# Optimization experiments

Hardware: AMD Instinct MI355X
Metric: run time of the kernel (lower is better)

The kernel has to match this reference:

```python
import jax, jax.numpy as jnp
import numpy as np

LEVEL = 2
INV_SQRT2 = 0.7071067811865476
# subband order: index 0 is the approx (x_coeff1[0]); the 7 details match the
# {'aad','ada','add','daa','dad','dda','ddd'} dict keys of wavedec3 level-`LEVEL`.
SUBS = ['aaa', 'aad', 'ada', 'add', 'daa', 'dad', 'dda', 'ddd']


def dwt1(x, axis):
    # single-level Haar (db1, periodic) analysis along one axis
    x = jnp.moveaxis(x, axis, -1)
    n = x.shape[-1]
    x = x.reshape(*x.shape[:-1], n // 2, 2)
    a = (x[..., 0] + x[..., 1]) * INV_SQRT2
    d = (x[..., 0] - x[..., 1]) * INV_SQRT2
    return jnp.moveaxis(a, -1, axis), jnp.moveaxis(d, -1, axis)


def dwt3(x):
    # separable 3D Haar DWT over the last 3 axes -> 8 subbands keyed 'aaa'..'ddd'
    subs = {'': x}
    for axis in (-3, -2, -1):
        nxt = {}
        for k, v in subs.items():
            a, d = dwt1(v, axis)
            nxt[k + 'a'] = a
            nxt[k + 'd'] = d
        subs = nxt
    return subs


def idwt1(a, d, axis):
    a = jnp.moveaxis(a, axis, -1)
    d = jnp.moveaxis(d, axis, -1)
    x = jnp.stack([(a + d) * INV_SQRT2, (a - d) * INV_SQRT2], axis=-1)
    x = x.reshape(*x.shape[:-2], x.shape[-2] * 2)
    return jnp.moveaxis(x, -1, axis)


def idwt3(subs):
    for axis in (-1, -2, -3):
        prefixes = sorted(set(k[:-1] for k in subs))
        subs = {p: idwt1(subs[p + 'a'], subs[p + 'd'], axis) for p in prefixes}
    return subs['']


def upsample_zero_details(a):
    # one inverse-DWT level with all detail coeffs = 0 (finer levels are zeroed
    # in the original forward for jj in 2..level)
    for axis in (-3, -2, -1):
        a = jnp.repeat(a, 2, axis=axis) * INV_SQRT2
    return a


def setup_inputs() -> dict:
    key = jax.random.key(0)
    k1, k2, k3, k4 = jax.random.split(key, 4)
    B, C, D, H, W = 4, 32, 64, 64, 64
    m = D >> LEVEL  # 16 = modes1
    scale = 1.0 / (C * C)
    x_1 = jax.random.normal(k1, (B, C, D, H, W), dtype=jnp.float32)
    x_2 = jax.random.normal(k2, (B, C, D, H, W), dtype=jnp.float32)
    W1 = scale * jax.random.uniform(k3, (8, C, C, m, m, m), dtype=jnp.float32)
    W2 = scale * jax.random.uniform(k4, (8, C, C, m, m, m), dtype=jnp.float32)
    return {'x_1': x_1, 'x_2': x_2, 'W1': W1, 'W2': W2}


def reference(x_1, x_2, W1, W2):
    # batched wavelet decompose -> per-subband channel mixing of the coarsest
    # level (the only level the original transforms; finer details are zeroed)
    a1, a2 = x_1, x_2
    for _ in range(LEVEL):
        s1 = dwt3(a1)
        s2 = dwt3(a2)
        a1 = s1['aaa']
        a2 = s2['aaa']
    mixed = {}
    for idx, k in enumerate(SUBS):
        mixed[k] = (jnp.einsum('bixyz,ioxyz->boxyz', s1[k], W1[idx])
                    + jnp.einsum('bixyz,ioxyz->boxyz', s2[k], W2[idx]))
    x = idwt3(mixed)  # level LEVEL -> LEVEL-1
    for _ in range(LEVEL - 1):
        x = upsample_zero_details(x)
    return x
```

## Files before the change

kernel.cpp:

```cpp
#include <hip/hip_runtime.h>


#define M3 4096
#define KS 524288
#define IS 4194304

__global__ __launch_bounds__(256, 4) void k_fwd(const float* __restrict__ x1,
                                                const float* __restrict__ x2,
                                                float* __restrict__ s) {
  const int tid = blockIdx.x * 256 + threadIdx.x;
  const int v    = tid & 4095;
  const int rest = tid >> 12;
  const int c   = rest & 31;
  const int b   = (rest >> 5) & 3;
  const int inp = rest >> 7;
  const float* __restrict__ X = inp ? x2 : x1;
  const int z = v & 15, y = (v >> 4) & 15, x = v >> 8;
  const float* base =
      X + ((((size_t)(b * 32 + c) * 64 + 4 * x) * 64 + 4 * y) * 64 + 4 * z);

  float4 f[16];
#pragma unroll
  for (int dd = 0; dd < 4; ++dd)
#pragma unroll
    for (int hh = 0; hh < 4; ++hh)
      f[dd * 4 + hh] = *reinterpret_cast<const float4*>(base + (dd * 64 + hh) * 64);

  float blk[2][2][2] = {{{0.f, 0.f}, {0.f, 0.f}}, {{0.f, 0.f}, {0.f, 0.f}}};
#pragma unroll
  for (int dd = 0; dd < 4; ++dd) {
#pragma unroll
    for (int hh = 0; hh < 4; ++hh) {
      const float4 t = f[dd * 4 + hh];
      blk[dd >> 1][hh >> 1][0] += t.x + t.y;
      blk[dd >> 1][hh >> 1][1] += t.z + t.w;
    }
  }
  const float a0 = blk[0][0][0], a1 = blk[0][0][1], a2 = blk[0][1][0], a3 = blk[0][1][1];
  const float a4 = blk[1][0][0], a5 = blk[1][0][1], a6 = blk[1][1][0], a7 = blk[1][1][1];
  const float t0 = a0 + a1, t1 = a0 - a1, t2 = a2 + a3, t3 = a2 - a3;
  const float t4 = a4 + a5, t5 = a4 - a5, t6 = a6 + a7, t7 = a6 - a7;
  const float u0 = t0 + t2, u2 = t0 - t2, u1 = t1 + t3, u3 = t1 - t3;
  const float u4 = t4 + t6, u6 = t4 - t6, u5 = t5 + t7, u7 = t5 - t7;
  float* o = s + (size_t)inp * IS + (size_t)(b * 32 + c) * M3 + v;
  o[0 * KS] = 0.125f * (u0 + u4);
  o[4 * KS] = 0.125f * (u0 - u4);
  o[1 * KS] = 0.125f * (u1 + u5);
  o[5 * KS] = 0.125f * (u1 - u5);
  o[2 * KS] = 0.125f * (u2 + u6);
  o[6 * KS] = 0.125f * (u2 - u6);
  o[3 * KS] = 0.125f * (u3 + u7);
  o[7 * KS] = 0.125f * (u3 - u7);
}

__global__ __launch_bounds__(256) void k_mix(const float* __restrict__ W1,
                                             const float* __restrict__ W2,
                                             const float* __restrict__ s,
                                             float* __restrict__ mixed) {
  const int bid  = blockIdx.x;
  const int k    = bid & 7;
  const int rest = bid >> 3;
  const int og   = rest & 3;
  const int vblk = rest >> 2;
  const int v = vblk * 256 + threadIdx.x;
  const float* pW1 = W1 + ((size_t)k * 1024 + og * 8) * M3 + v;
  const float* pW2 = W2 + ((size_t)k * 1024 + og * 8) * M3 + v;
  const float* ps  = s + (size_t)k * KS + v;
  float acc[4][8];
#pragma unroll
  for (int b = 0; b < 4; ++b)
#pragma unroll
    for (int oo = 0; oo < 8; ++oo) acc[b][oo] = 0.f;
#pragma unroll 2
  for (int i = 0; i < 32; ++i) {
    float s1b[4], s2b[4];
#pragma unroll
    for (int b = 0; b < 4; ++b) {
      s1b[b] = ps[(size_t)(b * 32 + i) * M3];
      s2b[b] = ps[(size_t)IS + (size_t)(b * 32 + i) * M3];
    }
#pragma unroll
    for (int oo = 0; oo < 8; ++oo) {
      const float w1 = pW1[(size_t)(i * 32 + oo) * M3];
      const float w2 = pW2[(size_t)(i * 32 + oo) * M3];
#pragma unroll
      for (int b = 0; b < 4; ++b) acc[b][oo] += s1b[b] * w1 + s2b[b] * w2;
    }
  }
  float* pm = mixed + (size_t)k * KS + (size_t)og * 8 * M3 + v;
#pragma unroll
  for (int b = 0; b < 4; ++b)
#pragma unroll
    for (int oo = 0; oo < 8; ++oo)
      pm[(size_t)b * (32 * M3) + (size_t)oo * M3] = acc[b][oo];
}

__global__ __launch_bounds__(256) void k_inv(const float* __restrict__ mixed,
                                             float* __restrict__ out) {
  const int tid = blockIdx.x * 256 + threadIdx.x;
  const int v = tid & 4095;
  const int o = (tid >> 12) & 31;
  const int b = tid >> 17;
  const float* pm = mixed + (size_t)(b * 32 + o) * M3 + v;
  const float m0 = pm[0 * (size_t)KS], m1 = pm[1 * (size_t)KS];
  const float m2 = pm[2 * (size_t)KS], m3 = pm[3 * (size_t)KS];
  const float m4 = pm[4 * (size_t)KS], m5 = pm[5 * (size_t)KS];
  const float m6 = pm[6 * (size_t)KS], m7 = pm[7 * (size_t)KS];
  const float t0 = m0 + m1, t1 = m0 - m1, t2 = m2 + m3, t3 = m2 - m3;
  const float t4 = m4 + m5, t5 = m4 - m5, t6 = m6 + m7, t7 = m6 - m7;
  const float u0 = t0 + t2, u2 = t0 - t2, u1 = t1 + t3, u3 = t1 - t3;
  const float u4 = t4 + t6, u6 = t4 - t6, u5 = t5 + t7, u7 = t5 - t7;
  float w[2][2][2];
  w[0][0][0] = 0.125f * (u0 + u4);
  w[1][0][0] = 0.125f * (u0 - u4);
  w[0][0][1] = 0.125f * (u1 + u5);
  w[1][0][1] = 0.125f * (u1 - u5);
  w[0][1][0] = 0.125f * (u2 + u6);
  w[1][1][0] = 0.125f * (u2 - u6);
  w[0][1][1] = 0.125f * (u3 + u7);
  w[1][1][1] = 0.125f * (u3 - u7);
  const int z = v & 15, y = (v >> 4) & 15, x = v >> 8;
  float* base =
      out + ((((size_t)(b * 32 + o) * 64 + 4 * x) * 64 + 4 * y) * 64 + 4 * z);
#pragma unroll
  for (int dd = 0; dd < 4; ++dd) {
    const int p = dd >> 1;
#pragma unroll
    for (int hh = 0; hh < 4; ++hh) {
      const int q = hh >> 1;
      const float lo = w[p][q][0], hi = w[p][q][1];
      float4 f;
      f.x = lo; f.y = lo; f.z = hi; f.w = hi;
      *reinterpret_cast<float4*>(base + (dd * 64 + hh) * 64) = f;
    }
  }
}

extern "C" void kernel_launch(void* const* d_in, const int* in_sizes, int n_in,
                              void* d_out, int out_size, void* d_ws, size_t ws_size,
                              hipStream_t stream) {
  const float* x1 = (const float*)d_in[0];
  const float* x2 = (const float*)d_in[1];
  const float* W1 = (const float*)d_in[2];
  const float* W2 = (const float*)d_in[3];
  float* out = (float*)d_out;
  float* s     = (float*)d_ws;
  float* mixed = s + 2 * (size_t)IS;
  k_fwd<<<4096, 256, 0, stream>>>(x1, x2, s);
  k_mix<<<512, 256, 0, stream>>>(W1, W2, s, mixed);
  k_inv<<<2048, 256, 0, stream>>>(mixed, out);
}
```

Baseline: 174.9 us.

## Coalesce forward DWT loads via shared-memory staging of pairwise sums

Each block of the forward-transform kernel now reads one contiguous 4x64x64 slab, so consecutive threads load consecutive float4s. Each thread pair-sums along z and writes the partial sums to padded shared memory. After a barrier, each thread gathers its 2x2x2 block from shared memory and finishes the Haar butterfly. Before, each thread's 64-float stride-64 access left neighbouring threads 16 bytes apart inside a row, with successive rows 256 bytes apart. The new scheme costs a shared-memory buffer and a __syncthreads, which may lower occupancy.

```diff
diff --git a/kernel.cpp b/kernel.cpp
--- a/kernel.cpp
+++ b/kernel.cpp
@@ -8,41 +8,58 @@
 __global__ __launch_bounds__(256, 4) void k_fwd(const float* __restrict__ x1,
                                                 const float* __restrict__ x2,
                                                 float* __restrict__ s) {
-  const int tid = blockIdx.x * 256 + threadIdx.x;
-  const int v    = tid & 4095;
-  const int rest = tid >> 12;
-  const int c   = rest & 31;
-  const int b   = (rest >> 5) & 3;
-  const int inp = rest >> 7;
-  const float* __restrict__ X = inp ? x2 : x1;
-  const int z = v & 15, y = (v >> 4) & 15, x = v >> 8;
-  const float* base =
-      X + ((((size_t)(b * 32 + c) * 64 + 4 * x) * 64 + 4 * y) * 64 + 4 * z);
+  const int bid  = blockIdx.x;
+  const int xsl  = bid & 15;
+  const int rest = bid >> 4;
+  const int bc   = rest & 127;
+  const int inp  = rest >> 7;
+  const float* __restrict__ X =
+      (inp ? x2 : x1) + (size_t)bc * 262144 + (size_t)xsl * 16384;
+
+  const int tid = threadIdx.x;
+  __shared__ float part[4 * 64 * 17 * 2];
 
   float4 f[16];
 #pragma unroll
-  for (int dd = 0; dd < 4; ++dd)
+  for (int j = 0; j < 16; ++j)
+    f[j] = *reinterpret_cast<const float4*>(X + j * 1024 + tid * 4);
+  __builtin_amdgcn_sched_barrier(0);
+
 #pragma unroll
-    for (int hh = 0; hh < 4; ++hh)
-      f[dd * 4 + hh] = *reinterpret_cast<const float4*>(base + (dd * 64 + hh) * 64);
+  for (int j = 0; j < 16; ++j) {
+    const int idx = j * 1024 + tid * 4;
+    const int d = idx >> 12;
+    const int h = (idx >> 6) & 63;
+    const int z = (idx & 63) >> 2;
+    float2 pr;
+    pr.x = f[j].x + f[j].y;
+    pr.y = f[j].z + f[j].w;
+    *reinterpret_cast<float2*>(&part[((d * 64 + h) * 17 + z) * 2]) = pr;
+  }
+  __syncthreads();
 
+  const int z = tid & 15, y = tid >> 4;
   float blk[2][2][2] = {{{0.f, 0.f}, {0.f, 0.f}}, {{0.f, 0.f}, {0.f, 0.f}}};
 #pragma unroll
-  for (int dd = 0; dd < 4; ++dd) {
+  for (int p = 0; p < 2; ++p)
 #pragma unroll
-    for (int hh = 0; hh < 4; ++hh) {
-      const float4 t = f[dd * 4 + hh];
-      blk[dd >> 1][hh >> 1][0] += t.x + t.y;
-      blk[dd >> 1][hh >> 1][1] += t.z + t.w;
-    }
-  }
+    for (int dd = 0; dd < 2; ++dd)
+#pragma unroll
+      for (int q = 0; q < 2; ++q)
+#pragma unroll
+        for (int hh = 0; hh < 2; ++hh) {
+          const float2 pr = *reinterpret_cast<const float2*>(
+              &part[(((2 * p + dd) * 64 + (4 * y + 2 * q + hh)) * 17 + z) * 2]);
+          blk[p][q][0] += pr.x;
+          blk[p][q][1] += pr.y;
+        }
   const float a0 = blk[0][0][0], a1 = blk[0][0][1], a2 = blk[0][1][0], a3 = blk[0][1][1];
   const float a4 = blk[1][0][0], a5 = blk[1][0][1], a6 = blk[1][1][0], a7 = blk[1][1][1];
   const float t0 = a0 + a1, t1 = a0 - a1, t2 = a2 + a3, t3 = a2 - a3;
   const float t4 = a4 + a5, t5 = a4 - a5, t6 = a6 + a7, t7 = a6 - a7;
   const float u0 = t0 + t2, u2 = t0 - t2, u1 = t1 + t3, u3 = t1 - t3;
   const float u4 = t4 + t6, u6 = t4 - t6, u5 = t5 + t7, u7 = t5 - t7;
-  float* o = s + (size_t)inp * IS + (size_t)(b * 32 + c) * M3 + v;
+  float* o = s + (size_t)inp * IS + (size_t)bc * M3 + xsl * 256 + y * 16 + z;
   o[0 * KS] = 0.125f * (u0 + u4);
   o[4 * KS] = 0.125f * (u0 - u4);
   o[1 * KS] = 0.125f * (u1 + u5);
```

After: 167.4 us. 1.04x faster.
